# Optimization experiments

Measured on AMD Instinct MI355X. Metric: run time of the kernel, lower is better.

## Reference

```python
import jax, jax.numpy as jnp
import numpy as np

D_MODEL = 1024
N_HEADS = 16
D_HEAD = D_MODEL // N_HEADS
WINDOW = 256
SCALE = D_HEAD ** -0.5


def setup_inputs() -> dict:
    key = jax.random.key(0)
    ks = jax.random.split(key, 5)
    B, S = 2, 2048
    x = jax.random.normal(ks[0], (B, S, D_MODEL), dtype=jnp.float32)
    # weights stored as [d_in, d_out] so forward is x @ W + b
    W_qkv = jax.random.normal(ks[1], (D_MODEL, 3 * D_MODEL), dtype=jnp.float32) * (D_MODEL ** -0.5)
    b_qkv = jnp.zeros((3 * D_MODEL,), dtype=jnp.float32)
    W_out = jax.random.normal(ks[2], (D_MODEL, D_MODEL), dtype=jnp.float32) * (D_MODEL ** -0.5)
    b_out = jnp.zeros((D_MODEL,), dtype=jnp.float32)
    return {"x": x, "W_qkv": W_qkv, "b_qkv": b_qkv, "W_out": W_out, "b_out": b_out}


def _window_mask(S):
    # Faithful to source: keep positions where (i <= j) & (i >= j - WINDOW + 1),
    # i = query index (rows), j = key index (cols). (Anti-causal window, as in repo.)
    idx = jnp.arange(S)
    keep = (idx[:, None] <= idx[None, :]) & (idx[:, None] >= idx[None, :] - WINDOW + 1)
    return keep  # [S, S] bool


def reference(x, W_qkv, b_qkv, W_out, b_out):
    B, S, D = x.shape
    qkv = x @ W_qkv + b_qkv                      # [B,S,3D]
    q, k, v = jnp.split(qkv, 3, axis=-1)
    def heads(t):
        return t.reshape(B, S, N_HEADS, D_HEAD).transpose(0, 2, 1, 3)  # [B,H,S,dh]
    q, k, v = heads(q), heads(k), heads(v)
    attn = jnp.einsum('bhid,bhjd->bhij', q, k) * SCALE  # [B,H,S,S]
    keep = _window_mask(S)
    attn = jnp.where(keep[None, None], attn, -jnp.inf)
    attn = jax.nn.softmax(attn, axis=-1)
    # dropout is identity in eval mode
    out = jnp.einsum('bhij,bhjd->bhid', attn, v)        # [B,H,S,dh]
    out = out.transpose(0, 2, 1, 3).reshape(B, S, D)
    return out @ W_out + b_out
```

## Files before the change

### kernel.cpp

```cpp
#include <hip/hip_runtime.h>

typedef __bf16 bf16x8 __attribute__((ext_vector_type(8)));
typedef float f32x4 __attribute__((ext_vector_type(4)));
typedef unsigned short u16x8 __attribute__((ext_vector_type(8)));
typedef unsigned short u16x4 __attribute__((ext_vector_type(4)));

#define MFMA16(a, b, c) __builtin_amdgcn_mfma_f32_16x16x32_bf16((a), (b), (c), 0, 0, 0)

__device__ __forceinline__ unsigned short f2bf(float f) {
  union { float f; unsigned int i; } v; v.f = f;
  unsigned int u = v.i;
  u += 0x7fffu + ((u >> 16) & 1u);
  return (unsigned short)(u >> 16);
}

__device__ __forceinline__ void gload16(const void* g, void* l) {
  __builtin_amdgcn_global_load_lds(
      (const __attribute__((address_space(1))) unsigned int*)g,
      (__attribute__((address_space(3))) unsigned int*)l, 16, 0, 0);
}

__global__ __launch_bounds__(256) void convert_x(const float* __restrict__ X,
                                                 unsigned short* __restrict__ Xb) {
  size_t i = (size_t)(blockIdx.x * 256 + threadIdx.x) * 8;
  f32x4 f0 = *(const f32x4*)(X + i);
  f32x4 f1 = *(const f32x4*)(X + i + 4);
  u16x8 t;
#pragma unroll
  for (int j = 0; j < 4; ++j) { t[j] = f2bf(f0[j]); t[4 + j] = f2bf(f1[j]); }
  *(u16x8*)(Xb + i) = t;
}

__global__ __launch_bounds__(256) void transpose_w(const float* __restrict__ W,
                                                   unsigned short* __restrict__ Wt,
                                                   int N) {
  __shared__ unsigned short t[32][33];
  int tx = threadIdx.x & 31, ty = threadIdx.x >> 5;
  int bx = blockIdx.x;
  int by = blockIdx.y;
#pragma unroll
  for (int j = 0; j < 4; ++j) {
    int r = ty + j * 8;
    t[tx][r] = f2bf(W[(size_t)(by * 32 + r) * N + bx * 32 + tx]);
  }
  __syncthreads();
#pragma unroll
  for (int j = 0; j < 4; ++j) {
    int r = ty + j * 8;
    Wt[(size_t)(bx * 32 + r) * 1024 + by * 32 + tx] = t[r][tx];
  }
}

__global__ __launch_bounds__(512) void gemm_bt(
    const unsigned short* __restrict__ A, const unsigned short* __restrict__ Bt,
    const float* __restrict__ bias,
    unsigned short* __restrict__ O0, unsigned short* __restrict__ O1,
    unsigned short* __restrict__ O2, float* __restrict__ OF, int mode) {
  __shared__ __align__(16) unsigned short As0[128 * 32];
  __shared__ __align__(16) unsigned short Bs0[128 * 32];
  __shared__ __align__(16) unsigned short As1[128 * 32];
  __shared__ __align__(16) unsigned short Bs1[128 * 32];

  const int K = 1024;
  int tid = threadIdx.x;
  int lane = tid & 63, wave = tid >> 6, quad = lane >> 4, l16 = lane & 15;
  int wr = wave >> 2, wc = wave & 3;
  int m0 = blockIdx.x * 128, n0 = blockIdx.y * 128;

  int srow = tid >> 2, su = tid & 3;
  const unsigned short* ag = A + (size_t)(m0 + srow) * K + su * 8;
  const unsigned short* bg = Bt + (size_t)(n0 + srow) * K + su * 8;
  int loff = tid * 16;

  int abase = (wr * 64 + l16) * 64 + quad * 16;
  int bbase = (wc * 32 + l16) * 64 + quad * 16;

  f32x4 acc[4][2];
#pragma unroll
  for (int i = 0; i < 4; ++i)
#pragma unroll
    for (int j = 0; j < 2; ++j) acc[i][j] = f32x4{0.f, 0.f, 0.f, 0.f};

  auto STAGE = [&](int k0, char* Asb, char* Bsb) {
    gload16(ag + k0, Asb + loff);
    gload16(bg + k0, Bsb + loff);
  };
  auto COMPUTE = [&](const char* Asb, const char* Bsb) {
    bf16x8 af[4], bfr[2];
#pragma unroll
    for (int t = 0; t < 4; ++t)
      af[t] = *(const bf16x8*)(Asb + abase + t * 1024);
#pragma unroll
    for (int t = 0; t < 2; ++t)
      bfr[t] = *(const bf16x8*)(Bsb + bbase + t * 1024);
#pragma unroll
    for (int mt = 0; mt < 4; ++mt)
#pragma unroll
      for (int nt = 0; nt < 2; ++nt)
        acc[mt][nt] = MFMA16(af[mt], bfr[nt], acc[mt][nt]);
  };
#define WAIT_VM2  asm volatile("s_waitcnt vmcnt(2)" ::: "memory")
#define WAIT_VM0  asm volatile("s_waitcnt vmcnt(0)" ::: "memory")
#define WAIT_LGKM asm volatile("s_waitcnt lgkmcnt(0)" ::: "memory")
#define BAR       __builtin_amdgcn_s_barrier()

  STAGE(0, (char*)As0, (char*)Bs0);
  for (int t = 0; t < 30; t += 2) {
    STAGE((t + 1) * 32, (char*)As1, (char*)Bs1);
    WAIT_VM2; BAR;
    COMPUTE((const char*)As0, (const char*)Bs0);
    WAIT_LGKM; BAR;
    STAGE((t + 2) * 32, (char*)As0, (char*)Bs0);
    WAIT_VM2; BAR;
    COMPUTE((const char*)As1, (const char*)Bs1);
    WAIT_LGKM; BAR;
  }
  STAGE(31 * 32, (char*)As1, (char*)Bs1);
  WAIT_VM2; BAR;
  COMPUTE((const char*)As0, (const char*)Bs0);
  WAIT_LGKM; BAR;
  WAIT_VM0; BAR;
  COMPUTE((const char*)As1, (const char*)Bs1);

  if (mode == 0) {
#pragma unroll
    for (int nt = 0; nt < 2; ++nt) {
      int n = n0 + wc * 32 + nt * 16 + l16;
      float bv = bias[n];
      int seg = n >> 10, cc = n & 1023, hh = cc >> 6, d = cc & 63;
#pragma unroll
      for (int mt = 0; mt < 4; ++mt) {
        int mb = m0 + wr * 64 + mt * 16 + quad * 4;
        int b = mb >> 11, s = mb & 2047;
        if (seg == 2) {
          u16x4 pk;
#pragma unroll
          for (int r = 0; r < 4; ++r) pk[r] = f2bf(acc[mt][nt][r] + bv);
          *(u16x4*)&O2[((size_t)((b << 4) + hh) * 64 + d) * 2048 + s] = pk;
        } else {
          unsigned short* O = seg ? O1 : O0;
#pragma unroll
          for (int r = 0; r < 4; ++r)
            O[((size_t)((b << 4) + hh) * 2048 + (s + r)) * 64 + d] = f2bf(acc[mt][nt][r] + bv);
        }
      }
    }
  } else {
#pragma unroll
    for (int nt = 0; nt < 2; ++nt) {
      int n = n0 + wc * 32 + nt * 16 + l16;
      float bv = bias[n];
#pragma unroll
      for (int mt = 0; mt < 4; ++mt) {
        int mb = m0 + wr * 64 + mt * 16 + quad * 4;
#pragma unroll
        for (int r = 0; r < 4; ++r)
          OF[(size_t)(mb + r) * 1024 + n] = acc[mt][nt][r] + bv;
      }
    }
  }
}

__global__ __launch_bounds__(256) void attn_kernel(
    const unsigned short* __restrict__ Q, const unsigned short* __restrict__ Kq,
    const unsigned short* __restrict__ Vt, unsigned short* __restrict__ AO) {
  __shared__ __align__(16) unsigned short Ks[32][72];
  __shared__ __align__(16) unsigned short Vs[64][40];
  __shared__ __align__(16) unsigned short Ps[4][16][40];

  int bid = blockIdx.x;
  int qblk = bid & 31, h = (bid >> 5) & 15, b = bid >> 9;
  int q0 = qblk * 64;
  int tid = threadIdx.x, lane = tid & 63, wave = tid >> 6, quad = lane >> 4, l16 = lane & 15;

  const unsigned short* Qb = Q + (size_t)(((b << 4) + h) * 2048) * 64;
  const unsigned short* Kb = Kq + (size_t)(((b << 4) + h) * 2048) * 64;
  const unsigned short* Vb = Vt + (size_t)(((b << 4) + h) * 64) * 2048;

  int qrow = q0 + wave * 16 + l16;
  bf16x8 qf0 = __builtin_bit_cast(bf16x8, *(const u16x8*)&Qb[(size_t)qrow * 64 + quad * 8]);
  bf16x8 qf1 = __builtin_bit_cast(bf16x8, *(const u16x8*)&Qb[(size_t)qrow * 64 + 32 + quad * 8]);

  float mrow[4], lrow[4];
  f32x4 zero = {0.f, 0.f, 0.f, 0.f};
  f32x4 o[4];
#pragma unroll
  for (int i = 0; i < 4; ++i) o[i] = zero;
#pragma unroll
  for (int r = 0; r < 4; ++r) { mrow[r] = -1e30f; lrow[r] = 0.f; }

  const float SCALE = 0.125f;
  int pstart = (wave >= 2) ? 1 : 0;
  int pend = pstart + 8;

  int ki = tid >> 3, kc = (tid & 7) * 8;
  int vd = tid >> 2, vc = (tid & 3) * 8;

  for (int p = 0; p < 10; ++p) {
    int kbase = q0 + p * 32;
    {
      int s = kbase + ki; s = s > 2047 ? 2047 : s;
      *(u16x8*)&Ks[ki][kc] = *(const u16x8*)&Kb[(size_t)s * 64 + kc];
    }
    if (kbase + vc + 7 <= 2047) {
      *(u16x8*)&Vs[vd][vc] = *(const u16x8*)&Vb[(size_t)vd * 2048 + kbase + vc];
    } else {
#pragma unroll
      for (int j = 0; j < 8; ++j) {
        int s = kbase + vc + j; s = s > 2047 ? 2047 : s;
        Vs[vd][vc + j] = Vb[(size_t)vd * 2048 + s];
      }
    }
    __syncthreads();

    if (p >= pstart && p <= pend) {
      f32x4 sc[2];
#pragma unroll
      for (int t = 0; t < 2; ++t) {
        bf16x8 kf0 = __builtin_bit_cast(bf16x8, *(const u16x8*)&Ks[t * 16 + l16][quad * 8]);
        bf16x8 kf1 = __builtin_bit_cast(bf16x8, *(const u16x8*)&Ks[t * 16 + l16][32 + quad * 8]);
        f32x4 z = zero;
        z = MFMA16(qf0, kf0, z);
        z = MFMA16(qf1, kf1, z);
        sc[t] = z;
      }
      float sv[2][4];
#pragma unroll
      for (int t = 0; t < 2; ++t)
#pragma unroll
        for (int r = 0; r < 4; ++r) {
          int kg = kbase + t * 16 + l16;
          int qg = q0 + wave * 16 + quad * 4 + r;
          bool valid = (kg >= qg) && (kg <= qg + 255) && (kg < 2048);
          sv[t][r] = valid ? sc[t][r] * SCALE : -1e30f;
        }
#pragma unroll
      for (int r = 0; r < 4; ++r) {
        float v = fmaxf(sv[0][r], sv[1][r]);
        v = fmaxf(v, __shfl_xor(v, 1));
        v = fmaxf(v, __shfl_xor(v, 2));
        v = fmaxf(v, __shfl_xor(v, 4));
        v = fmaxf(v, __shfl_xor(v, 8));
        float mnew = fmaxf(mrow[r], v);
        float alpha = __expf(mrow[r] - mnew);
        mrow[r] = mnew;
        float p0 = __expf(sv[0][r] - mnew);
        float p1 = __expf(sv[1][r] - mnew);
        p0 = (sv[0][r] > -5e29f) ? p0 : 0.f;
        p1 = (sv[1][r] > -5e29f) ? p1 : 0.f;
        float rs = p0 + p1;
        rs += __shfl_xor(rs, 1);
        rs += __shfl_xor(rs, 2);
        rs += __shfl_xor(rs, 4);
        rs += __shfl_xor(rs, 8);
        lrow[r] = lrow[r] * alpha + rs;
#pragma unroll
        for (int nt = 0; nt < 4; ++nt) o[nt][r] *= alpha;
        Ps[wave][quad * 4 + r][l16] = f2bf(p0);
        Ps[wave][quad * 4 + r][16 + l16] = f2bf(p1);
      }
      __threadfence_block();
      bf16x8 pf = __builtin_bit_cast(bf16x8, *(const u16x8*)&Ps[wave][l16][quad * 8]);
#pragma unroll
      for (int nt = 0; nt < 4; ++nt) {
        bf16x8 vf = __builtin_bit_cast(bf16x8, *(const u16x8*)&Vs[nt * 16 + l16][quad * 8]);
        o[nt] = MFMA16(pf, vf, o[nt]);
      }
    }
    __syncthreads();
  }

  unsigned short* dst = AO + ((size_t)(b * 2048 + q0 + wave * 16) * 1024) + h * 64;
#pragma unroll
  for (int nt = 0; nt < 4; ++nt)
#pragma unroll
    for (int r = 0; r < 4; ++r) {
      int qq = quad * 4 + r;
      dst[(size_t)qq * 1024 + nt * 16 + l16] = f2bf(o[nt][r] / lrow[r]);
    }
}

extern "C" void kernel_launch(void* const* d_in, const int* in_sizes, int n_in,
                              void* d_out, int out_size, void* d_ws, size_t ws_size,
                              hipStream_t stream) {
  const float* x = (const float*)d_in[0];
  const float* W_qkv = (const float*)d_in[1];
  const float* b_qkv = (const float*)d_in[2];
  const float* W_out = (const float*)d_in[3];
  const float* b_out = (const float*)d_in[4];
  float* out = (float*)d_out;

  unsigned short* ws = (unsigned short*)d_ws;
  unsigned short* Qw  = ws;
  unsigned short* Kw  = ws + 4194304;
  unsigned short* Vw  = ws + 8388608;
  unsigned short* Wqt = ws + 12582912;
  unsigned short* AO  = ws + 12582912;
  unsigned short* Wot = ws;
  unsigned short* Xb  = (unsigned short*)d_out;

  dim3 blk(256);
  dim3 gblk(512);
  convert_x<<<dim3(2048), blk, 0, stream>>>(x, Xb);
  transpose_w<<<dim3(96, 32), blk, 0, stream>>>(W_qkv, Wqt, 3072);
  gemm_bt<<<dim3(32, 24), gblk, 0, stream>>>(Xb, Wqt, b_qkv, Qw, Kw, Vw, nullptr, 0);
  attn_kernel<<<dim3(1024), blk, 0, stream>>>(Qw, Kw, Vw, AO);
  transpose_w<<<dim3(32, 32), blk, 0, stream>>>(W_out, Wot, 1024);
  gemm_bt<<<dim3(32, 8), gblk, 0, stream>>>(AO, Wot, b_out, nullptr, nullptr, nullptr, out, 1);
}
```

Measured before the change: 170.2 us.

## Load K/V fragments directly from global memory, dropping LDS staging and barriers

The attention kernel no longer stages K and V tiles cooperatively into shared memory behind two block-wide barriers per step. Each wave now loads its MFMA operand fragments straight from global memory and iterates only over its own key-block range, so waves run independently. `s_setprio` is raised around the MFMA sections. The cost is redundant global/L1 traffic, since all four waves fetch overlapping K/V data, and strided V loads that are not coalesced.

Result: slower. 174.1 us (+2.3%).

```diff
diff --git a/kernel.cpp b/kernel.cpp
--- a/kernel.cpp
+++ b/kernel.cpp
@@ -164,8 +164,6 @@
 __global__ __launch_bounds__(256) void attn_kernel(
     const unsigned short* __restrict__ Q, const unsigned short* __restrict__ Kq,
     const unsigned short* __restrict__ Vt, unsigned short* __restrict__ AO) {
-  __shared__ __align__(16) unsigned short Ks[32][72];
-  __shared__ __align__(16) unsigned short Vs[64][40];
   __shared__ __align__(16) unsigned short Ps[4][16][40];
 
   int bid = blockIdx.x;
@@ -193,81 +191,72 @@
   int pstart = (wave >= 2) ? 1 : 0;
   int pend = pstart + 8;
 
-  int ki = tid >> 3, kc = (tid & 7) * 8;
-  int vd = tid >> 2, vc = (tid & 3) * 8;
-
-  for (int p = 0; p < 10; ++p) {
+  for (int p = pstart; p <= pend; ++p) {
     int kbase = q0 + p * 32;
-    {
-      int s = kbase + ki; s = s > 2047 ? 2047 : s;
-      *(u16x8*)&Ks[ki][kc] = *(const u16x8*)&Kb[(size_t)s * 64 + kc];
-    }
-    if (kbase + vc + 7 <= 2047) {
-      *(u16x8*)&Vs[vd][vc] = *(const u16x8*)&Vb[(size_t)vd * 2048 + kbase + vc];
-    } else {
-#pragma unroll
-      for (int j = 0; j < 8; ++j) {
-        int s = kbase + vc + j; s = s > 2047 ? 2047 : s;
-        Vs[vd][vc + j] = Vb[(size_t)vd * 2048 + s];
+
+    f32x4 sc[2];
+    __builtin_amdgcn_s_setprio(1);
+#pragma unroll
+    for (int t = 0; t < 2; ++t) {
+      int krow = kbase + t * 16 + l16;
+      krow = krow > 2047 ? 2047 : krow;
+      bf16x8 kf0 = __builtin_bit_cast(bf16x8, *(const u16x8*)&Kb[(size_t)krow * 64 + quad * 8]);
+      bf16x8 kf1 = __builtin_bit_cast(bf16x8, *(const u16x8*)&Kb[(size_t)krow * 64 + 32 + quad * 8]);
+      f32x4 z = zero;
+      z = MFMA16(qf0, kf0, z);
+      z = MFMA16(qf1, kf1, z);
+      sc[t] = z;
+    }
+    __builtin_amdgcn_s_setprio(0);
+
+    float sv[2][4];
+#pragma unroll
+    for (int t = 0; t < 2; ++t)
+#pragma unroll
+      for (int r = 0; r < 4; ++r) {
+        int kg = kbase + t * 16 + l16;
+        int qg = q0 + wave * 16 + quad * 4 + r;
+        bool valid = (kg >= qg) && (kg <= qg + 255) && (kg < 2048);
+        sv[t][r] = valid ? sc[t][r] * SCALE : -1e30f;
       }
-    }
-    __syncthreads();
-
-    if (p >= pstart && p <= pend) {
-      f32x4 sc[2];
-#pragma unroll
-      for (int t = 0; t < 2; ++t) {
-        bf16x8 kf0 = __builtin_bit_cast(bf16x8, *(const u16x8*)&Ks[t * 16 + l16][quad * 8]);
-        bf16x8 kf1 = __builtin_bit_cast(bf16x8, *(const u16x8*)&Ks[t * 16 + l16][32 + quad * 8]);
-        f32x4 z = zero;
-        z = MFMA16(qf0, kf0, z);
-        z = MFMA16(qf1, kf1, z);
-        sc[t] = z;
-      }
-      float sv[2][4];
-#pragma unroll
-      for (int t = 0; t < 2; ++t)
-#pragma unroll
-        for (int r = 0; r < 4; ++r) {
-          int kg = kbase + t * 16 + l16;
-          int qg = q0 + wave * 16 + quad * 4 + r;
-          bool valid = (kg >= qg) && (kg <= qg + 255) && (kg < 2048);
-          sv[t][r] = valid ? sc[t][r] * SCALE : -1e30f;
-        }
-#pragma unroll
-      for (int r = 0; r < 4; ++r) {
-        float v = fmaxf(sv[0][r], sv[1][r]);
-        v = fmaxf(v, __shfl_xor(v, 1));
-        v = fmaxf(v, __shfl_xor(v, 2));
-        v = fmaxf(v, __shfl_xor(v, 4));
-        v = fmaxf(v, __shfl_xor(v, 8));
-        float mnew = fmaxf(mrow[r], v);
-        float alpha = __expf(mrow[r] - mnew);
-        mrow[r] = mnew;
-        float p0 = __expf(sv[0][r] - mnew);
-        float p1 = __expf(sv[1][r] - mnew);
-        p0 = (sv[0][r] > -5e29f) ? p0 : 0.f;
-        p1 = (sv[1][r] > -5e29f) ? p1 : 0.f;
-        float rs = p0 + p1;
-        rs += __shfl_xor(rs, 1);
-        rs += __shfl_xor(rs, 2);
-        rs += __shfl_xor(rs, 4);
-        rs += __shfl_xor(rs, 8);
-        lrow[r] = lrow[r] * alpha + rs;
-#pragma unroll
-        for (int nt = 0; nt < 4; ++nt) o[nt][r] *= alpha;
-        Ps[wave][quad * 4 + r][l16] = f2bf(p0);
-        Ps[wave][quad * 4 + r][16 + l16] = f2bf(p1);
-      }
-      __threadfence_block();
-      bf16x8 pf = __builtin_bit_cast(bf16x8, *(const u16x8*)&Ps[wave][l16][quad * 8]);
-#pragma unroll
-      for (int nt = 0; nt < 4; ++nt) {
-        bf16x8 vf = __builtin_bit_cast(bf16x8, *(const u16x8*)&Vs[nt * 16 + l16][quad * 8]);
-        o[nt] = MFMA16(pf, vf, o[nt]);
-      }
-    }
-    __syncthreads();
+#pragma unroll
+    for (int r = 0; r < 4; ++r) {
+      float v = fmaxf(sv[0][r], sv[1][r]);
+      v = fmaxf(v, __shfl_xor(v, 1));
+      v = fmaxf(v, __shfl_xor(v, 2));
+      v = fmaxf(v, __shfl_xor(v, 4));
+      v = fmaxf(v, __shfl_xor(v, 8));
+      float mnew = fmaxf(mrow[r], v);
+      float alpha = __expf(mrow[r] - mnew);
+      mrow[r] = mnew;
+      float p0 = __expf(sv[0][r] - mnew);
+      float p1 = __expf(sv[1][r] - mnew);
+      p0 = (sv[0][r] > -5e29f) ? p0 : 0.f;
+      p1 = (sv[1][r] > -5e29f) ? p1 : 0.f;
+      float rs = p0 + p1;
+      rs += __shfl_xor(rs, 1);
+      rs += __shfl_xor(rs, 2);
+      rs += __shfl_xor(rs, 4);
+      rs += __shfl_xor(rs, 8);
+      lrow[r] = lrow[r] * alpha + rs;
+#pragma unroll
+      for (int nt = 0; nt < 4; ++nt) o[nt][r] *= alpha;
+      Ps[wave][quad * 4 + r][l16] = f2bf(p0);
+      Ps[wave][quad * 4 + r][16 + l16] = f2bf(p1);
+    }
+    __threadfence_block();
+    bf16x8 pf = __builtin_bit_cast(bf16x8, *(const u16x8*)&Ps[wave][l16][quad * 8]);
+
+    int vcol = kbase + quad * 8;
+    vcol = vcol > 2040 ? 2040 : vcol;
+    __builtin_amdgcn_s_setprio(1);
+#pragma unroll
+    for (int nt = 0; nt < 4; ++nt) {
+      int vrow = nt * 16 + l16;
+      bf16x8 vf = __builtin_bit_cast(bf16x8, *(const u16x8*)&Vb[(size_t)vrow * 2048 + vcol]);
+      o[nt] = MFMA16(pf, vf, o[nt]);
+    }
+    __builtin_amdgcn_s_setprio(0);
   }
 
   unsigned short* dst = AO + ((size_t)(b * 2048 + q0 + wave * 16) * 1024) + h * 64;
```
